# Performance work log

Hardware: AMD Instinct MI355X
Metric: run time of the kernel (lower is better)

Reference implementation:

```python
import jax, jax.numpy as jnp
import numpy as np

DIMS = 1024
HEAD = 16
HD = DIMS // HEAD          # head_dim = 64
LAYER = 2
STRIDE = max(1, 6 - LAYER)  # skip-path k/v stride = 4
EPS = 1.1920929e-07         # torch.finfo(float32).eps (RMSNorm eps=None default)


def rmsnorm(x, w):
    # torch nn.RMSNorm over last dim with affine weight
    ms = jnp.mean(jnp.square(x), axis=-1, keepdims=True)
    return x * jax.lax.rsqrt(ms + EPS) * w


def rope_freqs(seq_len):
    # rotary._compute_freqs with mask=None, x=None (mel-style scale)
    end = 2595.0 * np.log10(1.0 + 4000.0 / 200.0)
    scale = jnp.power(10.0, jnp.linspace(0.0, end, HD // 2, dtype=jnp.float32) / 2595.0) - 1.0
    base = 200.0 * scale / 1000.0                      # [HD//2]
    t = jnp.arange(seq_len, dtype=jnp.float32)          # [c]
    return t[:, None] * base[None, :]                   # [c, HD//2]


def rope(x, freqs):
    # x: [b,h,c,d]; interleaved pairs rotated by angle freqs[c, d//2]
    xr = x.reshape(*x.shape[:-1], HD // 2, 2)
    a, b = xr[..., 0], xr[..., 1]
    cos, sin = jnp.cos(freqs), jnp.sin(freqs)           # broadcast over [b,h]
    out = jnp.stack([a * cos - b * sin, a * sin + b * cos], axis=-1)
    return out.reshape(x.shape)


def setup_inputs() -> dict:
    key = jax.random.key(0)
    ks = jax.random.split(key, 4)
    d = DIMS
    init = lambda k, shape: jax.random.normal(k, shape, jnp.float32) * 0.02
    return {
        "x": jax.random.normal(ks[0], (4, 2048, d), jnp.float32),
        "rmsq_w": jnp.ones((d,), jnp.float32),
        "q_w": init(ks[1], (d, d)),
        "q_b": jnp.zeros((d,), jnp.float32),
        "rmskv_w": jnp.ones((d,), jnp.float32),
        "kv_w": init(ks[2], (d, 2 * d)),
        "kv_b": jnp.zeros((2 * d,), jnp.float32),
        "ln_w": jnp.ones((HD,), jnp.float32),
        "out_w": init(ks[3], (d, d)),
        "out_b": jnp.zeros((d,), jnp.float32),
    }


def reference(x, rmsq_w, q_w, q_b, rmskv_w, kv_w, kv_b, ln_w, out_w, out_b):
    b, c, d = x.shape
    # q = RMSNorm -> Linear -> [b,h,c,hd]
    q = (rmsnorm(x, rmsq_w) @ q_w + q_b).reshape(b, c, HEAD, HD).transpose(0, 2, 1, 3)
    # kv = RMSNorm -> Linear(d,2d) -> split last dim as (kv=2, h, hd)
    kv = (rmsnorm(x, rmskv_w) @ kv_w + kv_b).reshape(b, c, 2, HEAD, HD)
    k = kv[:, :, 0].transpose(0, 2, 1, 3)  # [b,h,c,hd]
    v = kv[:, :, 1].transpose(0, 2, 1, 3)
    # rotary embedding (full hd rotated since freqs cover hd//2 pairs)
    freqs = rope_freqs(c)
    q = rope(q, freqs)
    k = rope(k, freqs)
    # skip branch: strided subsampling of k/v (stride = max(1, 6-layer) = 4)
    k = k[:, :, ::STRIDE, :]
    v = v[:, :, ::STRIDE, :]
    # per-head RMSNorm on q/k, then SDPA (is_causal=False since mask=None)
    qn = rmsnorm(q, ln_w)
    kn = rmsnorm(k, ln_w)
    scores = jnp.einsum('bhqd,bhkd->bhqk', qn, kn) / jnp.sqrt(jnp.float32(HD))
    a = jnp.einsum('bhqk,bhkd->bhqd', jax.nn.softmax(scores, axis=-1), v)
    # out projection: [b,h,c,hd] -> [b,c,d] -> Linear
    out = a.transpose(0, 2, 1, 3).reshape(b, c, d) @ out_w + out_b
    return out
```

## Files before the change

kernel.cpp:

```cpp
#include <hip/hip_runtime.h>

#define EPSF 1.1920929e-07f
#define QSCALE 0.18033688011112042f

typedef _Float16 hf;
typedef __attribute__((ext_vector_type(4))) _Float16 h4;
typedef __attribute__((ext_vector_type(4))) float fx4;

#define DEVI __device__ __forceinline__

DEVI void async16(const void* g, void* l) {
  __builtin_amdgcn_global_load_lds((const __attribute__((address_space(1))) unsigned int*)g,
                                   (__attribute__((address_space(3))) unsigned int*)l, 16, 0, 0);
}

DEVI fx4 mfma16(h4 a, h4 b, fx4 c) {
  return __builtin_amdgcn_mfma_f32_16x16x16f16(a, b, c, 0, 0, 0);
}

DEVI h4 ldfrag(const hf* base, int row, int g) {
  int off = row * 128 + ((g ^ ((row & 7) << 1)) << 3);
  return *(const h4*)((const char*)base + off);
}

__global__ __launch_bounds__(256) void k_wcast(const float* __restrict__ W, hf* __restrict__ Wt,
                                               int K, int N) {
  __shared__ float ls[64][65];
  int kt = blockIdx.x, nt = blockIdx.y, t = threadIdx.x;
  int c4 = (t & 15) * 4, r0 = t >> 4;
#pragma unroll
  for (int i = 0; i < 4; ++i) {
    int row = i * 16 + r0;
    fx4 v = *(const fx4*)(W + (size_t)(kt * 64 + row) * N + nt * 64 + c4);
    ls[row][c4 + 0] = v[0]; ls[row][c4 + 1] = v[1];
    ls[row][c4 + 2] = v[2]; ls[row][c4 + 3] = v[3];
  }
  __syncthreads();
  int cc = t >> 4, kk4 = (t & 15) * 4;
#pragma unroll
  for (int i = 0; i < 4; ++i) {
    int nn = i * 16 + cc;
    h4 p = {(hf)ls[kk4 + 0][nn], (hf)ls[kk4 + 1][nn], (hf)ls[kk4 + 2][nn], (hf)ls[kk4 + 3][nn]};
    *(h4*)(Wt + (size_t)(nt * 64 + nn) * K + kt * 64 + kk4) = p;
  }
}

__global__ __launch_bounds__(256) void k_table(float* __restrict__ tab) {
  int idx = blockIdx.x * 256 + threadIdx.x;
  int tt = idx >> 5, j = idx & 31;
  double e = pow(21.0, (double)j / 31.0) - 1.0;
  float bf = (float)(0.2 * e);
  float fr = (float)tt * bf;
  double d = (double)fr;
  float2 cs = make_float2((float)cos(d), (float)sin(d));
  ((float2*)tab)[idx] = cs;
}

__global__ __launch_bounds__(256) void k_dualnorm(const float* __restrict__ x,
                                                  const float* __restrict__ wq,
                                                  const float* __restrict__ wkv,
                                                  hf* __restrict__ xqn, hf* __restrict__ xkvc) {
  int row = blockIdx.x, t = threadIdx.x;
  const fx4* xr = (const fx4*)(x + (size_t)row * 1024);
  fx4 v = xr[t];
  float ss = v[0] * v[0] + v[1] * v[1] + v[2] * v[2] + v[3] * v[3];
#pragma unroll
  for (int m = 1; m <= 32; m <<= 1) ss += __shfl_xor(ss, m);
  __shared__ float red[4];
  if ((t & 63) == 0) red[t >> 6] = ss;
  __syncthreads();
  float r = rsqrtf((red[0] + red[1] + red[2] + red[3]) * (1.0f / 1024.0f) + EPSF);
  fx4 a = ((const fx4*)wq)[t];
  h4 oq = {(hf)(v[0] * r * a[0]), (hf)(v[1] * r * a[1]), (hf)(v[2] * r * a[2]), (hf)(v[3] * r * a[3])};
  *(h4*)(xqn + (size_t)row * 1024 + t * 4) = oq;
  int c = row & 2047;
  if ((c & 3) == 0) {
    fx4 bk = ((const fx4*)wkv)[t];
    int crow = (row >> 11) * 512 + (c >> 2);
    h4 ok = {(hf)(v[0] * r * bk[0]), (hf)(v[1] * r * bk[1]), (hf)(v[2] * r * bk[2]), (hf)(v[3] * r * bk[3])};
    *(h4*)(xkvc + (size_t)crow * 1024 + t * 4) = ok;
  }
}

template <int EPI>
__global__ __launch_bounds__(256) void k_gemm(const hf* __restrict__ A, const hf* __restrict__ Bt,
                                              const float* __restrict__ bias, void* __restrict__ outp,
                                              int M, int N, int K, int MB, hf* __restrict__ vt) {
  __shared__ hf lsA[128 * 64];
  __shared__ hf lsB[128 * 64];
  int t = threadIdx.x, l = t & 63, w = t >> 6, grp = l >> 4, ln = l & 15;
  int bm = blockIdx.x % MB, bn = blockIdx.x / MB;
  int m0 = bm * 128, n0 = bn * 128;
  int wr = w >> 1, wc = w & 1;
  fx4 acc[4][4] = {};
  int nkt = K >> 6;
  for (int kt = 0; kt < nkt; ++kt) {
    int k0 = kt << 6;
    __syncthreads();
#pragma unroll
    for (int p = 0; p < 4; ++p) {
      int ci = p * 256 + w * 64 + l;
      int row = ci >> 3, cc = ci & 7;
      int sw = (cc ^ (row & 7)) * 8;
      async16(A + (size_t)(m0 + row) * K + k0 + sw, (char*)lsA + p * 4096 + w * 1024);
      async16(Bt + (size_t)(n0 + row) * K + k0 + sw, (char*)lsB + p * 4096 + w * 1024);
    }
    __syncthreads();
#pragma unroll
    for (int kk = 0; kk < 4; ++kk) {
      h4 af[4], bf[4];
#pragma unroll
      for (int i = 0; i < 4; ++i) af[i] = ldfrag(lsA, wr * 64 + i * 16 + ln, kk * 4 + grp);
#pragma unroll
      for (int i = 0; i < 4; ++i) bf[i] = ldfrag(lsB, wc * 64 + i * 16 + ln, kk * 4 + grp);
#pragma unroll
      for (int mi = 0; mi < 4; ++mi)
#pragma unroll
        for (int ni = 0; ni < 4; ++ni)
          acc[mi][ni] = mfma16(af[mi], bf[ni], acc[mi][ni]);
    }
  }
#pragma unroll
  for (int ni = 0; ni < 4; ++ni) {
    int n = n0 + wc * 64 + ni * 16 + ln;
    float bs = bias[n];
#pragma unroll
    for (int mi = 0; mi < 4; ++mi) {
      int mb_ = m0 + wr * 64 + mi * 16 + grp * 4;
      fx4 v = acc[mi][ni];
      v += bs;
      if constexpr (EPI == 2) {
        float* O = (float*)outp;
#pragma unroll
        for (int r = 0; r < 4; ++r) O[(size_t)(mb_ + r) * N + n] = v[r];
      } else if constexpr (EPI == 0) {
        hf* O = (hf*)outp;
#pragma unroll
        for (int r = 0; r < 4; ++r) O[(size_t)(mb_ + r) * N + n] = (hf)v[r];
      } else {
        if (n < 1024) {
          hf* O = (hf*)outp;
#pragma unroll
          for (int r = 0; r < 4; ++r) O[(size_t)(mb_ + r) * 1024 + n] = (hf)v[r];
        } else {
          int nv = n - 1024, h = nv >> 6, hd = nv & 63;
          int b = m0 >> 9, kc0 = mb_ & 511;
          h4 pk = {(hf)v[0], (hf)v[1], (hf)v[2], (hf)v[3]};
          *(h4*)(vt + ((size_t)(b * 16 + h) * 64 + hd) * 512 + kc0) = pk;
        }
      }
    }
  }
}

template <bool ISQ>
__global__ __launch_bounds__(256) void k_post(const hf* __restrict__ raw, const float* __restrict__ lnw,
                                              const float* __restrict__ tab, hf* __restrict__ outn) {
  int row = blockIdx.x, t = threadIdx.x;
  int h = t >> 4, hd0 = (t & 15) * 4;
  h4 q = ((const h4*)(raw + (size_t)row * 1024))[t];
  float q0 = (float)q[0], q1 = (float)q[1], q2 = (float)q[2], q3 = (float)q[3];
  float ss = q0 * q0 + q1 * q1 + q2 * q2 + q3 * q3;
  ss += __shfl_xor(ss, 1); ss += __shfl_xor(ss, 2);
  ss += __shfl_xor(ss, 4); ss += __shfl_xor(ss, 8);
  float scl = rsqrtf(ss * (1.0f / 64.0f) + EPSF);
  if (ISQ) scl *= QSCALE;
  int b, c, seq;
  if (ISQ) { b = row >> 11; c = row & 2047; seq = c; }
  else     { b = row >> 9;  c = row & 511;  seq = c * 4; }
  fx4 cs = *(const fx4*)(tab + (size_t)seq * 64 + hd0);
  float o0 = q0 * cs[0] - q1 * cs[1];
  float o1 = q0 * cs[1] + q1 * cs[0];
  float o2 = q2 * cs[2] - q3 * cs[3];
  float o3 = q2 * cs[3] + q3 * cs[2];
  fx4 lw = *(const fx4*)(lnw + hd0);
  h4 o = {(hf)(o0 * lw[0] * scl), (hf)(o1 * lw[1] * scl), (hf)(o2 * lw[2] * scl), (hf)(o3 * lw[3] * scl)};
  int rows = ISQ ? 2048 : 512;
  *(h4*)(outn + ((size_t)(b * 16 + h) * rows + c) * 64 + hd0) = o;
}

__global__ __launch_bounds__(256) void k_attn(const hf* __restrict__ qn, const hf* __restrict__ kn,
                                              const hf* __restrict__ vt, hf* __restrict__ a) {
  __shared__ hf lsK[64 * 64];
  __shared__ hf lsV[64 * 64];
  int t = threadIdx.x, l = t & 63, w = t >> 6, grp = l >> 4, ln = l & 15;
  int bq = blockIdx.x & 15, plane = blockIdx.x >> 4;
  const hf* qp = qn + (size_t)plane * 2048 * 64;
  const hf* kp = kn + (size_t)plane * 512 * 64;
  const hf* vp = vt + (size_t)plane * 64 * 512;
  int q0 = bq * 128 + w * 32;

  h4 qf[2][4];
#pragma unroll
  for (int mf = 0; mf < 2; ++mf)
#pragma unroll
    for (int kk = 0; kk < 4; ++kk)
      qf[mf][kk] = *(const h4*)(qp + (size_t)(q0 + mf * 16 + ln) * 64 + kk * 16 + grp * 4);

  fx4 o[4][2] = {};
  float mrun[2] = {-1e30f, -1e30f}, lrun[2] = {0.f, 0.f};

  for (int ch = 0; ch < 8; ++ch) {
    int kc0 = ch * 64;
    __syncthreads();
#pragma unroll
    for (int p = 0; p < 2; ++p) {
      int ci = p * 256 + w * 64 + l;
      int key = ci >> 3, cc = ci & 7;
      async16(kp + (size_t)(kc0 + key) * 64 + ((cc ^ (key & 7)) * 8), (char*)lsK + p * 4096 + w * 1024);
    }
#pragma unroll
    for (int p = 0; p < 2; ++p) {
      int ci = p * 256 + w * 64 + l;
      int hd = ci >> 3, cc = ci & 7;
      async16(vp + (size_t)hd * 512 + kc0 + ((cc ^ (hd & 7)) * 8), (char*)lsV + p * 4096 + w * 1024);
    }
    __syncthreads();

    fx4 s[4][2] = {};
#pragma unroll
    for (int kk = 0; kk < 4; ++kk) {
      h4 kf[4];
#pragma unroll
      for (int kt = 0; kt < 4; ++kt) kf[kt] = ldfrag(lsK, kt * 16 + ln, kk * 4 + grp);
#pragma unroll
      for (int kt = 0; kt < 4; ++kt)
#pragma unroll
        for (int mf = 0; mf < 2; ++mf)
          s[kt][mf] = mfma16(kf[kt], qf[mf][kk], s[kt][mf]);
    }

    float al[2];
#pragma unroll
    for (int mf = 0; mf < 2; ++mf) {
      float cm = -1e30f;
#pragma unroll
      for (int kt = 0; kt < 4; ++kt) {
        fx4 sv = s[kt][mf];
        cm = fmaxf(cm, fmaxf(fmaxf(sv[0], sv[1]), fmaxf(sv[2], sv[3])));
      }
      cm = fmaxf(cm, __shfl_xor(cm, 16));
      cm = fmaxf(cm, __shfl_xor(cm, 32));
      float mn = fmaxf(mrun[mf], cm);
      al[mf] = exp2f(mrun[mf] - mn);
      mrun[mf] = mn;
    }
    float ps[2] = {0.f, 0.f};
#pragma unroll
    for (int kt = 0; kt < 4; ++kt)
#pragma unroll
      for (int mf = 0; mf < 2; ++mf)
#pragma unroll
        for (int j = 0; j < 4; ++j) {
          float pv = exp2f(s[kt][mf][j] - mrun[mf]);
          s[kt][mf][j] = pv;
          ps[mf] += pv;
        }
#pragma unroll
    for (int mf = 0; mf < 2; ++mf) {
      ps[mf] += __shfl_xor(ps[mf], 16);
      ps[mf] += __shfl_xor(ps[mf], 32);
      lrun[mf] = lrun[mf] * al[mf] + ps[mf];
    }
#pragma unroll
    for (int nh = 0; nh < 4; ++nh)
#pragma unroll
      for (int mf = 0; mf < 2; ++mf) o[nh][mf] *= al[mf];

    h4 pf[4][2];
#pragma unroll
    for (int kt = 0; kt < 4; ++kt)
#pragma unroll
      for (int mf = 0; mf < 2; ++mf) {
        fx4 sv = s[kt][mf];
        h4 tmp = {(hf)sv[0], (hf)sv[1], (hf)sv[2], (hf)sv[3]};
        pf[kt][mf] = tmp;
      }
#pragma unroll
    for (int ks = 0; ks < 4; ++ks) {
      h4 vf[4];
#pragma unroll
      for (int nh = 0; nh < 4; ++nh) vf[nh] = ldfrag(lsV, nh * 16 + ln, ks * 4 + grp);
#pragma unroll
      for (int nh = 0; nh < 4; ++nh)
#pragma unroll
        for (int mf = 0; mf < 2; ++mf)
          o[nh][mf] = mfma16(vf[nh], pf[ks][mf], o[nh][mf]);
    }
  }

  int b = plane >> 4, h = plane & 15;
#pragma unroll
  for (int mf = 0; mf < 2; ++mf) {
    float inv = 1.0f / lrun[mf];
    int cpos = q0 + mf * 16 + ln;
    size_t rowo = ((size_t)b * 2048 + cpos) * 1024;
#pragma unroll
    for (int nh = 0; nh < 4; ++nh) {
      h4 pk = {(hf)(o[nh][mf][0] * inv), (hf)(o[nh][mf][1] * inv),
               (hf)(o[nh][mf][2] * inv), (hf)(o[nh][mf][3] * inv)};
      *(h4*)(a + rowo + h * 64 + nh * 16 + grp * 4) = pk;
    }
  }
}

extern "C" void kernel_launch(void* const* d_in, const int* in_sizes, int n_in,
                              void* d_out, int out_size, void* d_ws, size_t ws_size,
                              hipStream_t stream) {
  (void)in_sizes; (void)n_in; (void)out_size; (void)ws_size;
  const float* x      = (const float*)d_in[0];
  const float* rmsq_w = (const float*)d_in[1];
  const float* q_w    = (const float*)d_in[2];
  const float* q_b    = (const float*)d_in[3];
  const float* rmskv_w= (const float*)d_in[4];
  const float* kv_w   = (const float*)d_in[5];
  const float* kv_b   = (const float*)d_in[6];
  const float* ln_w   = (const float*)d_in[7];
  const float* out_w  = (const float*)d_in[8];
  const float* out_b  = (const float*)d_in[9];

  char* ws = (char*)d_ws;
  hf* wqT   = (hf*)(ws + (size_t)0);
  hf* wkvT  = (hf*)(ws + ((size_t)2 << 20));
  hf* woT   = (hf*)(ws + ((size_t)6 << 20));
  float* tab= (float*)(ws + ((size_t)8 << 20));
  hf* xqn   = (hf*)(ws + ((size_t)9 << 20));
  hf* qn    = xqn;
  hf* xkvc  = (hf*)(ws + ((size_t)25 << 20));
  hf* qraw  = (hf*)(ws + ((size_t)29 << 20));
  hf* abuf  = qraw;
  hf* kraw  = (hf*)(ws + ((size_t)45 << 20));
  hf* kn    = (hf*)(ws + ((size_t)49 << 20));
  hf* vt    = (hf*)(ws + ((size_t)53 << 20));

  k_wcast<<<dim3(16, 16), 256, 0, stream>>>(q_w,   wqT,  1024, 1024);
  k_wcast<<<dim3(16, 32), 256, 0, stream>>>(kv_w,  wkvT, 1024, 2048);
  k_wcast<<<dim3(16, 16), 256, 0, stream>>>(out_w, woT,  1024, 1024);
  k_table<<<256, 256, 0, stream>>>(tab);
  k_dualnorm<<<8192, 256, 0, stream>>>(x, rmsq_w, rmskv_w, xqn, xkvc);
  k_gemm<0><<<64 * 8, 256, 0, stream>>>(xqn, wqT, q_b, qraw, 8192, 1024, 1024, 64, nullptr);
  k_gemm<1><<<16 * 16, 256, 0, stream>>>(xkvc, wkvT, kv_b, kraw, 2048, 2048, 1024, 16, vt);
  k_post<true><<<8192, 256, 0, stream>>>(qraw, ln_w, tab, qn);
  k_post<false><<<2048, 256, 0, stream>>>(kraw, ln_w, tab, kn);
  k_attn<<<1024, 256, 0, stream>>>(qn, kn, vt, abuf);
  k_gemm<2><<<64 * 8, 256, 0, stream>>>(abuf, woT, out_b, d_out, 8192, 1024, 1024, 64, nullptr);
}
```

Baseline: 268.2 us.

## Double-buffer LDS tiles, use 16x16x32 MFMA, and add lazy softmax rescaling

The GEMM and attention kernels now keep two LDS buffers and prefetch the next K or V tile asynchronously while computing on the current one. This removes one barrier per iteration and hides global load latency. The QK and GEMM inner loops switch to the 16x16x32 f16 MFMA with 8-wide fragment loads. Attention also skips the online-softmax rescale unless the running max grows by more than 8 and uses the raw exp2 builtin. The cost is double the LDS use, which may lower occupancy, and some numerical slack in the softmax.

```diff
diff --git a/kernel.cpp b/kernel.cpp
--- a/kernel.cpp
+++ b/kernel.cpp
@@ -5,6 +5,7 @@
 
 typedef _Float16 hf;
 typedef __attribute__((ext_vector_type(4))) _Float16 h4;
+typedef __attribute__((ext_vector_type(8))) _Float16 h8;
 typedef __attribute__((ext_vector_type(4))) float fx4;
 
 #define DEVI __device__ __forceinline__
@@ -17,9 +18,16 @@
 DEVI fx4 mfma16(h4 a, h4 b, fx4 c) {
   return __builtin_amdgcn_mfma_f32_16x16x16f16(a, b, c, 0, 0, 0);
 }
-
-DEVI h4 ldfrag(const hf* base, int row, int g) {
-  int off = row * 128 + ((g ^ ((row & 7) << 1)) << 3);
+DEVI fx4 mfma32(h8 a, h8 b, fx4 c) {
+  return __builtin_amdgcn_mfma_f32_16x16x32_f16(a, b, c, 0, 0, 0);
+}
+
+DEVI h8 ld16(const hf* base, int row, int g16) {
+  int off = (row * 128 + (g16 << 4)) ^ ((row & 7) << 4);
+  return *(const h8*)((const char*)base + off);
+}
+DEVI h4 ld8(const hf* base, int row, int g8) {
+  int off = (row * 128 + (g8 << 3)) ^ ((row & 7) << 4);
   return *(const h4*)((const char*)base + off);
 }
 
@@ -86,39 +94,51 @@
 __global__ __launch_bounds__(256) void k_gemm(const hf* __restrict__ A, const hf* __restrict__ Bt,
                                               const float* __restrict__ bias, void* __restrict__ outp,
                                               int M, int N, int K, int MB, hf* __restrict__ vt) {
-  __shared__ hf lsA[128 * 64];
-  __shared__ hf lsB[128 * 64];
+  __shared__ alignas(16) hf lsA[2][128 * 64];
+  __shared__ alignas(16) hf lsB[2][128 * 64];
   int t = threadIdx.x, l = t & 63, w = t >> 6, grp = l >> 4, ln = l & 15;
   int bm = blockIdx.x % MB, bn = blockIdx.x / MB;
   int m0 = bm * 128, n0 = bn * 128;
   int wr = w >> 1, wc = w & 1;
   fx4 acc[4][4] = {};
   int nkt = K >> 6;
+
+  auto stage = [&](int kt, int b) {
+    int k0 = kt << 6;
+#pragma unroll
+    for (int p = 0; p < 4; ++p) {
+      int ci = p * 256 + t;
+      int row = ci >> 3, g = (ci & 7) ^ (row & 7);
+      async16(A + (size_t)(m0 + row) * K + k0 + g * 8, (char*)lsA[b] + p * 4096 + w * 1024);
+    }
+#pragma unroll
+    for (int p = 0; p < 4; ++p) {
+      int ci = p * 256 + t;
+      int row = ci >> 3, g = (ci & 7) ^ (row & 7);
+      async16(Bt + (size_t)(n0 + row) * K + k0 + g * 8, (char*)lsB[b] + p * 4096 + w * 1024);
+    }
+  };
+
+  stage(0, 0);
+  __syncthreads();
   for (int kt = 0; kt < nkt; ++kt) {
-    int k0 = kt << 6;
+    int cur = kt & 1;
+    if (kt + 1 < nkt) stage(kt + 1, cur ^ 1);
+    __builtin_amdgcn_sched_barrier(0);
+#pragma unroll
+    for (int kk = 0; kk < 2; ++kk) {
+      h8 af[4], bf[4];
+#pragma unroll
+      for (int i = 0; i < 4; ++i) af[i] = ld16(lsA[cur], wr * 64 + i * 16 + ln, kk * 4 + grp);
+#pragma unroll
+      for (int i = 0; i < 4; ++i) bf[i] = ld16(lsB[cur], wc * 64 + i * 16 + ln, kk * 4 + grp);
+#pragma unroll
+      for (int mi = 0; mi < 4; ++mi)
+#pragma unroll
+        for (int ni = 0; ni < 4; ++ni)
+          acc[mi][ni] = mfma32(af[mi], bf[ni], acc[mi][ni]);
+    }
     __syncthreads();
-#pragma unroll
-    for (int p = 0; p < 4; ++p) {
-      int ci = p * 256 + w * 64 + l;
-      int row = ci >> 3, cc = ci & 7;
-      int sw = (cc ^ (row & 7)) * 8;
-      async16(A + (size_t)(m0 + row) * K + k0 + sw, (char*)lsA + p * 4096 + w * 1024);
-      async16(Bt + (size_t)(n0 + row) * K + k0 + sw, (char*)lsB + p * 4096 + w * 1024);
-    }
-    __syncthreads();
-#pragma unroll
-    for (int kk = 0; kk < 4; ++kk) {
-      h4 af[4], bf[4];
-#pragma unroll
-      for (int i = 0; i < 4; ++i) af[i] = ldfrag(lsA, wr * 64 + i * 16 + ln, kk * 4 + grp);
-#pragma unroll
-      for (int i = 0; i < 4; ++i) bf[i] = ldfrag(lsB, wc * 64 + i * 16 + ln, kk * 4 + grp);
-#pragma unroll
-      for (int mi = 0; mi < 4; ++mi)
-#pragma unroll
-        for (int ni = 0; ni < 4; ++ni)
-          acc[mi][ni] = mfma16(af[mi], bf[ni], acc[mi][ni]);
-    }
   }
 #pragma unroll
   for (int ni = 0; ni < 4; ++ni) {
@@ -181,8 +201,8 @@
 
 __global__ __launch_bounds__(256) void k_attn(const hf* __restrict__ qn, const hf* __restrict__ kn,
                                               const hf* __restrict__ vt, hf* __restrict__ a) {
-  __shared__ hf lsK[64 * 64];
-  __shared__ hf lsV[64 * 64];
+  __shared__ alignas(16) hf lsK[2][64 * 64];
+  __shared__ alignas(16) hf lsV[2][64 * 64];
   int t = threadIdx.x, l = t & 63, w = t >> 6, grp = l >> 4, ln = l & 15;
   int bq = blockIdx.x & 15, plane = blockIdx.x >> 4;
   const hf* qp = qn + (size_t)plane * 2048 * 64;
@@ -190,103 +210,108 @@
   const hf* vp = vt + (size_t)plane * 64 * 512;
   int q0 = bq * 128 + w * 32;
 
-  h4 qf[2][4];
+  h8 qf[2][2];
 #pragma unroll
   for (int mf = 0; mf < 2; ++mf)
 #pragma unroll
-    for (int kk = 0; kk < 4; ++kk)
-      qf[mf][kk] = *(const h4*)(qp + (size_t)(q0 + mf * 16 + ln) * 64 + kk * 16 + grp * 4);
+    for (int kk = 0; kk < 2; ++kk)
+      qf[mf][kk] = *(const h8*)(qp + (size_t)(q0 + mf * 16 + ln) * 64 + kk * 32 + grp * 8);
 
   fx4 o[4][2] = {};
   float mrun[2] = {-1e30f, -1e30f}, lrun[2] = {0.f, 0.f};
 
+  auto stageKV = [&](int ch, int b) {
+    int kc0 = ch * 64;
+#pragma unroll
+    for (int p = 0; p < 2; ++p) {
+      int ci = p * 256 + t;
+      int row = ci >> 3, g = (ci & 7) ^ (row & 7);
+      async16(kp + (size_t)(kc0 + row) * 64 + g * 8, (char*)lsK[b] + p * 4096 + w * 1024);
+    }
+#pragma unroll
+    for (int p = 0; p < 2; ++p) {
+      int ci = p * 256 + t;
+      int row = ci >> 3, g = (ci & 7) ^ (row & 7);
+      async16(vp + (size_t)row * 512 + kc0 + g * 8, (char*)lsV[b] + p * 4096 + w * 1024);
+    }
+  };
+
+  stageKV(0, 0);
+  __syncthreads();
+
   for (int ch = 0; ch < 8; ++ch) {
-    int kc0 = ch * 64;
-    __syncthreads();
-#pragma unroll
-    for (int p = 0; p < 2; ++p) {
-      int ci = p * 256 + w * 64 + l;
-      int key = ci >> 3, cc = ci & 7;
-      async16(kp + (size_t)(kc0 + key) * 64 + ((cc ^ (key & 7)) * 8), (char*)lsK + p * 4096 + w * 1024);
-    }
-#pragma unroll
-    for (int p = 0; p < 2; ++p) {
-      int ci = p * 256 + w * 64 + l;
-      int hd = ci >> 3, cc = ci & 7;
-      async16(vp + (size_t)hd * 512 + kc0 + ((cc ^ (hd & 7)) * 8), (char*)lsV + p * 4096 + w * 1024);
-    }
-    __syncthreads();
+    int cur = ch & 1;
+    if (ch < 7) stageKV(ch + 1, cur ^ 1);
+    __builtin_amdgcn_sched_barrier(0);
 
     fx4 s[4][2] = {};
 #pragma unroll
-    for (int kk = 0; kk < 4; ++kk) {
-      h4 kf[4];
-#pragma unroll
-      for (int kt = 0; kt < 4; ++kt) kf[kt] = ldfrag(lsK, kt * 16 + ln, kk * 4 + grp);
+    for (int kk = 0; kk < 2; ++kk) {
+      h8 kf[4];
+#pragma unroll
+      for (int kt = 0; kt < 4; ++kt) kf[kt] = ld16(lsK[cur], kt * 16 + ln, kk * 4 + grp);
 #pragma unroll
       for (int kt = 0; kt < 4; ++kt)
 #pragma unroll
         for (int mf = 0; mf < 2; ++mf)
-          s[kt][mf] = mfma16(kf[kt], qf[mf][kk], s[kt][mf]);
-    }
-
-    float al[2];
+          s[kt][mf] = mfma32(kf[kt], qf[mf][kk], s[kt][mf]);
+    }
+
 #pragma unroll
     for (int mf = 0; mf < 2; ++mf) {
       float cm = -1e30f;
 #pragma unroll
       for (int kt = 0; kt < 4; ++kt) {
         fx4 sv = s[kt][mf];
-        cm = fmaxf(cm, fmaxf(fmaxf(sv[0], sv[1]), fmaxf(sv[2], sv[3])));
+        cm = fmaxf(fmaxf(cm, fmaxf(sv[0], sv[1])), fmaxf(sv[2], sv[3]));
       }
       cm = fmaxf(cm, __shfl_xor(cm, 16));
       cm = fmaxf(cm, __shfl_xor(cm, 32));
-      float mn = fmaxf(mrun[mf], cm);
-      al[mf] = exp2f(mrun[mf] - mn);
-      mrun[mf] = mn;
-    }
+      if (__any(cm > mrun[mf] + 8.0f)) {
+        float mn = fmaxf(mrun[mf], cm);
+        float al = __builtin_amdgcn_exp2f(mrun[mf] - mn);
+        mrun[mf] = mn;
+        lrun[mf] *= al;
+#pragma unroll
+        for (int nh = 0; nh < 4; ++nh) o[nh][mf] *= al;
+      }
+    }
+
     float ps[2] = {0.f, 0.f};
-#pragma unroll
-    for (int kt = 0; kt < 4; ++kt)
-#pragma unroll
-      for (int mf = 0; mf < 2; ++mf)
-#pragma unroll
-        for (int j = 0; j < 4; ++j) {
-          float pv = exp2f(s[kt][mf][j] - mrun[mf]);
-          s[kt][mf][j] = pv;
-          ps[mf] += pv;
-        }
-#pragma unroll
-    for (int mf = 0; mf < 2; ++mf) {
-      ps[mf] += __shfl_xor(ps[mf], 16);
-      ps[mf] += __shfl_xor(ps[mf], 32);
-      lrun[mf] = lrun[mf] * al[mf] + ps[mf];
-    }
-#pragma unroll
-    for (int nh = 0; nh < 4; ++nh)
-#pragma unroll
-      for (int mf = 0; mf < 2; ++mf) o[nh][mf] *= al[mf];
-
     h4 pf[4][2];
 #pragma unroll
     for (int kt = 0; kt < 4; ++kt)
 #pragma unroll
       for (int mf = 0; mf < 2; ++mf) {
         fx4 sv = s[kt][mf];
-        h4 tmp = {(hf)sv[0], (hf)sv[1], (hf)sv[2], (hf)sv[3]};
-        pf[kt][mf] = tmp;
+        float e0 = __builtin_amdgcn_exp2f(sv[0] - mrun[mf]);
+        float e1 = __builtin_amdgcn_exp2f(sv[1] - mrun[mf]);
+        float e2 = __builtin_amdgcn_exp2f(sv[2] - mrun[mf]);
+        float e3 = __builtin_amdgcn_exp2f(sv[3] - mrun[mf]);
+        ps[mf] += (e0 + e1) + (e2 + e3);
+        h4 tp = {(hf)e0, (hf)e1, (hf)e2, (hf)e3};
+        pf[kt][mf] = tp;
       }
+#pragma unroll
+    for (int mf = 0; mf < 2; ++mf) {
+      float p2 = ps[mf];
+      p2 += __shfl_xor(p2, 16);
+      p2 += __shfl_xor(p2, 32);
+      lrun[mf] += p2;
+    }
+
 #pragma unroll
     for (int ks = 0; ks < 4; ++ks) {
       h4 vf[4];
 #pragma unroll
-      for (int nh = 0; nh < 4; ++nh) vf[nh] = ldfrag(lsV, nh * 16 + ln, ks * 4 + grp);
+      for (int nh = 0; nh < 4; ++nh) vf[nh] = ld8(lsV[cur], nh * 16 + ln, ks * 4 + grp);
 #pragma unroll
       for (int nh = 0; nh < 4; ++nh)
 #pragma unroll
         for (int mf = 0; mf < 2; ++mf)
           o[nh][mf] = mfma16(vf[nh], pf[ks][mf], o[nh][mf]);
     }
+    __syncthreads();
   }
 
   int b = plane >> 4, h = plane & 15;
```

Result: faster. 233.4 us (-13.0%).
